# Optimization experiments

Measured on AMD Instinct MI355X. Metric: run time of the kernel, lower is better.

## Reference

```python
import jax, jax.numpy as jnp
import numpy as np

NUM_ACTIONS = 16  # number of unique leaf actions (= output_dim)


def setup_inputs() -> dict:
    key = jax.random.key(0)
    ks = jax.random.split(key, 7)
    B, IN, D, A = 32768, 128, 511, 512
    L = D + A + 1  # 1024 leaves
    x = jax.random.normal(ks[0], (B, IN), dtype=jnp.float32)
    Wd = jax.random.normal(ks[1], (D, IN), dtype=jnp.float32) * 0.05
    bd = jax.random.normal(ks[2], (D,), dtype=jnp.float32) * 0.05
    Wa = jax.random.normal(ks[3], (A, IN), dtype=jnp.float32) * 0.05
    ba = jax.random.normal(ks[4], (A,), dtype=jnp.float32) * 0.05
    Wl = jax.random.normal(ks[5], (L, 2 * (D + A)), dtype=jnp.float32) * 0.05
    seg_ids = jax.random.randint(ks[6], (L,), 0, NUM_ACTIONS, dtype=jnp.int32)
    return {"x": x, "Wd": Wd, "bd": bd, "Wa": Wa, "ba": ba, "Wl": Wl,
            "seg_ids": seg_ids}


def reference(x, Wd, bd, Wa, ba, Wl, seg_ids):
    # dual linear heads (torch Linear: y = x @ W.T + b)
    x1 = x @ Wd.T + bd            # [B, D]
    x2 = x @ Wa.T + ba            # [B, A]
    h = jnp.concatenate([x1, x2], axis=1)                     # [B, D+A]
    hh = jnp.concatenate([jax.nn.relu(h), jax.nn.relu(-h)], axis=1)  # [B, 2(D+A)]
    leaf = hh @ Wl.T              # [B, L]
    # ragged per-action max over leaf columns (MaxPoolLayer)
    pooled = jax.ops.segment_max(leaf.T, seg_ids,
                                 num_segments=NUM_ACTIONS).T   # [B, NUM_ACTIONS]
    return jax.nn.softmax(pooled, axis=-1)
```

## Files before the change

kernel.cpp:

```cpp
#include <hip/hip_runtime.h>
#include <hip/hip_bf16.h>
#include <cstdint>
#include <cmath>

#define AS1 __attribute__((address_space(1)))
#define AS3 __attribute__((address_space(3)))

typedef unsigned short u16;
typedef uint32_t u32;
typedef __attribute__((ext_vector_type(8))) __bf16 bf16x8;
typedef __attribute__((ext_vector_type(8))) unsigned short u16x8;
typedef __attribute__((ext_vector_type(4))) float f32x4;

__device__ __forceinline__ u16 f2bf(float f) {
    uint32_t u = __builtin_bit_cast(uint32_t, f);
    return (u16)((u + 0x7fffu + ((u >> 16) & 1u)) >> 16);
}

__device__ __forceinline__ u32 f2ord(float f) {
    u32 u = __builtin_bit_cast(u32, f);
    return u ^ (u32)(((int32_t)u >> 31) | 0x80000000);
}
__device__ __forceinline__ float ord2f(u32 v) {
    u32 u = (v & 0x80000000u) ? (v ^ 0x80000000u) : ~v;
    return __builtin_bit_cast(float, u);
}

__global__ void setup_all(const float* __restrict__ x,
                          const float* __restrict__ Wd, const float* __restrict__ bd,
                          const float* __restrict__ Wa, const float* __restrict__ ba,
                          const float* __restrict__ Wl,
                          u16* __restrict__ xb, u16* __restrict__ w1b,
                          float* __restrict__ bb, u16* __restrict__ w1t,
                          u16* __restrict__ wsb, u16* __restrict__ dlb,
                          float* __restrict__ cl) {
    __shared__ float cred[256];
    const int b = blockIdx.x;
    const int tid = threadIdx.x;
    if (b < 2048) {
        long idx = (long)(b * 256 + tid) * 8;
        float4 a = *(const float4*)(x + idx);
        float4 c = *(const float4*)(x + idx + 4);
        u16x8 o;
        o[0]=f2bf(a.x); o[1]=f2bf(a.y); o[2]=f2bf(a.z); o[3]=f2bf(a.w);
        o[4]=f2bf(c.x); o[5]=f2bf(c.y); o[6]=f2bf(c.z); o[7]=f2bf(c.w);
        *(u16x8*)(xb + idx) = o;
    } else if (b < 2112) {
        int t = (b - 2048) * 256 + tid;
        int row = t >> 4, g = (t & 15) * 8;
        const float* src = nullptr;
        if (row < 511)       src = Wd + row * 128 + g;
        else if (row < 1023) src = Wa + (row - 511) * 128 + g;
        u16x8 o = 0;
        if (src) {
            #pragma unroll
            for (int j = 0; j < 8; ++j) o[j] = f2bf(src[j]);
        }
        *(u16x8*)(w1b + row * 128 + g) = o;
        #pragma unroll
        for (int j = 0; j < 8; ++j) w1t[(g + j) * 1024 + row] = o[j];
        if ((t & 15) == 0)
            bb[row] = row < 511 ? bd[row] : (row < 1023 ? ba[row - 511] : 0.f);
    } else {
        const int l0 = (b - 2112) * 2;
        const int lo = tid >> 7, g = (tid & 127) * 8;
        const float* src = Wl + (long)(l0 + lo) * 2046;
        u16x8 os, od;
        float part = 0.f;
        #pragma unroll
        for (int j = 0; j < 8; ++j) {
            int c = g + j;
            float pa = 0.f, pb = 0.f;
            if (c < 1023) { pa = src[c]; pb = src[1023 + c]; }
            os[j] = f2bf(0.5f * (pa + pb));
            float v = pa - pb;
            od[j] = f2bf(v);
            float b1 = c < 511 ? bd[c] : (c < 1023 ? ba[c - 511] : 0.f);
            part += v * b1;
        }
        *(u16x8*)(wsb + (long)(l0 + lo) * 1024 + g) = os;
        *(u16x8*)(dlb + (long)(l0 + lo) * 1024 + g) = od;
        cred[tid] = part;
        __syncthreads();
        if (tid < 2) {
            float s = 0.f;
            #pragma unroll
            for (int k = 0; k < 128; ++k) s += cred[tid * 128 + k];
            cl[l0 + tid] = 0.5f * s;
        }
    }
}

__global__ __launch_bounds__(256) void gemm_hwc(
        const u16* __restrict__ xb, const u16* __restrict__ w1b,
        const float* __restrict__ bb,
        const u16* __restrict__ dlb, const u16* __restrict__ w1t,
        u16* __restrict__ habs, u16* __restrict__ wcb) {
    __shared__ union SharedU {
        struct { u16 As[2][4096]; u16 Bs[2][4096]; } s;
        u16 obuf[128 * 132];
    } sh;
    const int tid  = threadIdx.x;
    const int lane = tid & 63, wave = tid >> 6;
    const int wy = wave >> 1, wx = wave & 1;
    const int i16 = lane & 15, q = lane >> 4;
    const int cA = wave * 2, srow = lane >> 2, scol = (lane & 3) * 8;

    f32x4 acc[4][4];
    #pragma unroll
    for (int m = 0; m < 4; ++m)
        #pragma unroll
        for (int n = 0; n < 4; ++n) acc[m][n] = f32x4{0.f,0.f,0.f,0.f};

    if (blockIdx.y == 0) {
        const long blockM = (long)blockIdx.x * 128;
        const int koff = (blockIdx.x * 4) & 31;
        const u16* a0 = dlb + (blockM + cA * 16 + srow) * 1024 + scol;
        const u16* a1 = dlb + (blockM + (cA + 1) * 16 + srow) * 1024 + scol;
        const u16* b0 = w1t + (long)(cA * 16 + srow) * 1024 + scol;
        const u16* b1 = w1t + (long)((cA + 1) * 16 + srow) * 1024 + scol;
        for (int it = 0; it < 32; ++it) {
            const int k0 = ((it + koff) & 31) << 5;
            __builtin_amdgcn_global_load_lds((const AS1 void*)(a0 + k0), (AS3 void*)&sh.s.As[0][cA * 512],       16, 0, 0);
            __builtin_amdgcn_global_load_lds((const AS1 void*)(a1 + k0), (AS3 void*)&sh.s.As[0][(cA + 1) * 512], 16, 0, 0);
            __builtin_amdgcn_global_load_lds((const AS1 void*)(b0 + k0), (AS3 void*)&sh.s.Bs[0][cA * 512],       16, 0, 0);
            __builtin_amdgcn_global_load_lds((const AS1 void*)(b1 + k0), (AS3 void*)&sh.s.Bs[0][(cA + 1) * 512], 16, 0, 0);
            __syncthreads();
            bf16x8 af[4], bfv[4];
            #pragma unroll
            for (int s = 0; s < 4; ++s) {
                af[s]  = *(const bf16x8*)&sh.s.As[0][(wy * 64 + s * 16 + i16) * 32 + q * 8];
                bfv[s] = *(const bf16x8*)&sh.s.Bs[0][(wx * 64 + s * 16 + i16) * 32 + q * 8];
            }
            #pragma unroll
            for (int sm = 0; sm < 4; ++sm)
                #pragma unroll
                for (int sn = 0; sn < 4; ++sn)
                    acc[sm][sn] = __builtin_amdgcn_mfma_f32_16x16x32_bf16(af[sm], bfv[sn], acc[sm][sn], 0, 0, 0);
            __syncthreads();
        }
        #pragma unroll
        for (int sm = 0; sm < 4; ++sm)
            #pragma unroll
            for (int sn = 0; sn < 4; ++sn) {
                const int col = wx * 64 + sn * 16 + i16;
                #pragma unroll
                for (int r = 0; r < 4; ++r) {
                    const long row = blockM + wy * 64 + sm * 16 + 4 * q + r;
                    wcb[row * 128 + col] = f2bf(0.5f * acc[sm][sn][r]);
                }
            }
        return;
    }

    const int xcd = blockIdx.x, yy = blockIdx.y - 1;
    const long blockM = (long)(xcd * 32 + (yy >> 3)) * 128;
    const int  blockN = (yy & 7) * 128;
    const int  koff = (yy >> 3) & 1;

    const u16* a0 = xb + (blockM + cA * 16 + srow) * 128 + scol;
    const u16* a1 = xb + (blockM + (cA + 1) * 16 + srow) * 128 + scol;
    const u16* b0 = w1b + ((long)blockN + cA * 16 + srow) * 128 + scol;
    const u16* b1 = w1b + ((long)blockN + (cA + 1) * 16 + srow) * 128 + scol;
    for (int it = 0; it < 2; ++it) {
        const int k0 = ((it + koff) & 1) << 6;
        #pragma unroll
        for (int p = 0; p < 2; ++p) {
            const int kp = k0 + p * 32;
            __builtin_amdgcn_global_load_lds((const AS1 void*)(a0 + kp), (AS3 void*)&sh.s.As[p][cA * 512],       16, 0, 0);
            __builtin_amdgcn_global_load_lds((const AS1 void*)(a1 + kp), (AS3 void*)&sh.s.As[p][(cA + 1) * 512], 16, 0, 0);
            __builtin_amdgcn_global_load_lds((const AS1 void*)(b0 + kp), (AS3 void*)&sh.s.Bs[p][cA * 512],       16, 0, 0);
            __builtin_amdgcn_global_load_lds((const AS1 void*)(b1 + kp), (AS3 void*)&sh.s.Bs[p][(cA + 1) * 512], 16, 0, 0);
        }
        __syncthreads();
        #pragma unroll
        for (int p = 0; p < 2; ++p) {
            bf16x8 af[4], bfv[4];
            #pragma unroll
            for (int s = 0; s < 4; ++s) {
                af[s]  = *(const bf16x8*)&sh.s.As[p][(wy * 64 + s * 16 + i16) * 32 + q * 8];
                bfv[s] = *(const bf16x8*)&sh.s.Bs[p][(wx * 64 + s * 16 + i16) * 32 + q * 8];
            }
            #pragma unroll
            for (int sm = 0; sm < 4; ++sm)
                #pragma unroll
                for (int sn = 0; sn < 4; ++sn)
                    acc[sm][sn] = __builtin_amdgcn_mfma_f32_16x16x32_bf16(af[sm], bfv[sn], acc[sm][sn], 0, 0, 0);
        }
        __syncthreads();
    }

    float bv[4];
    #pragma unroll
    for (int sn = 0; sn < 4; ++sn) bv[sn] = bb[blockN + wx * 64 + sn * 16 + i16];
    #pragma unroll
    for (int sm = 0; sm < 4; ++sm)
        #pragma unroll
        for (int sn = 0; sn < 4; ++sn)
            #pragma unroll
            for (int r = 0; r < 4; ++r)
                sh.obuf[(wy * 64 + sm * 16 + 4 * q + r) * 132 + wx * 64 + sn * 16 + i16] =
                    f2bf(fabsf(acc[sm][sn][r] + bv[sn]));
    __syncthreads();
    const int cg = (tid & 15) * 8;
    #pragma unroll
    for (int it = 0; it < 8; ++it) {
        const int row = it * 16 + (tid >> 4);
        *(u16x8*)&habs[(blockM + row) * 1024 + blockN + cg] =
            *(const u16x8*)&sh.obuf[row * 132 + cg];
    }
}

__global__ __launch_bounds__(256) void gemm_leaf(const u16* __restrict__ habs,
        const u16* __restrict__ xb, const u16* __restrict__ wsb,
        const u16* __restrict__ wcb, const float* __restrict__ cl,
        const int* __restrict__ seg, u32* __restrict__ pp) {
    __shared__ u16 As[2][128 * 32];
    __shared__ u16 Bs[2][128 * 32];
    __shared__ u32 pmax[128 * 16];
    const int tid  = threadIdx.x;
    const int lane = tid & 63, wave = tid >> 6;
    const int wy = wave >> 1, wx = wave & 1;
    const int i16 = lane & 15, q = lane >> 4;
    const int xcd = blockIdx.x, y = blockIdx.y;
    const int nTile = y & 7;
    const long blockM = (long)(xcd * 32 + (y >> 3)) * 128;
    const int  blockN = nTile * 128;
    const int  koff = ((y >> 3) * 2) & 15;

    #pragma unroll
    for (int j = 0; j < 8; ++j) pmax[tid + j * 256] = 0u;

    f32x4 acc[4][4];
    #pragma unroll
    for (int m = 0; m < 4; ++m)
        #pragma unroll
        for (int n = 0; n < 4; ++n) acc[m][n] = f32x4{0.f,0.f,0.f,0.f};

    const int cA = wave * 2, srow = lane >> 2, scol = (lane & 3) * 8;
    {
        const u16* a0 = habs + (blockM + cA * 16 + srow) * 1024 + scol;
        const u16* a1 = habs + (blockM + (cA + 1) * 16 + srow) * 1024 + scol;
        const u16* b0 = wsb + ((long)blockN + cA * 16 + srow) * 1024 + scol;
        const u16* b1 = wsb + ((long)blockN + (cA + 1) * 16 + srow) * 1024 + scol;
        auto kstep = [&](int k0) {
            #pragma unroll
            for (int p = 0; p < 2; ++p) {
                const int kp = k0 + p * 32;
                __builtin_amdgcn_global_load_lds((const AS1 void*)(a0 + kp), (AS3 void*)&As[p][cA * 512],       16, 0, 0);
                __builtin_amdgcn_global_load_lds((const AS1 void*)(a1 + kp), (AS3 void*)&As[p][(cA + 1) * 512], 16, 0, 0);
                __builtin_amdgcn_global_load_lds((const AS1 void*)(b0 + kp), (AS3 void*)&Bs[p][cA * 512],       16, 0, 0);
                __builtin_amdgcn_global_load_lds((const AS1 void*)(b1 + kp), (AS3 void*)&Bs[p][(cA + 1) * 512], 16, 0, 0);
            }
            __syncthreads();
            #pragma unroll
            for (int p = 0; p < 2; ++p) {
                bf16x8 af[4], bfv[4];
                #pragma unroll
                for (int s = 0; s < 4; ++s) {
                    af[s]  = *(const bf16x8*)&As[p][(wy * 64 + s * 16 + i16) * 32 + q * 8];
                    bfv[s] = *(const bf16x8*)&Bs[p][(wx * 64 + s * 16 + i16) * 32 + q * 8];
                }
                #pragma unroll
                for (int sm = 0; sm < 4; ++sm)
                    #pragma unroll
                    for (int sn = 0; sn < 4; ++sn)
                        acc[sm][sn] = __builtin_amdgcn_mfma_f32_16x16x32_bf16(af[sm], bfv[sn], acc[sm][sn], 0, 0, 0);
            }
            __syncthreads();
        };
        for (int it = koff; it < 16; ++it) kstep(it << 6);
        for (int it = 0; it < koff; ++it)  kstep(it << 6);
    }
    {
        const u16* a0 = xb + (blockM + cA * 16 + srow) * 128 + scol;
        const u16* a1 = xb + (blockM + (cA + 1) * 16 + srow) * 128 + scol;
        const u16* b0 = wcb + ((long)blockN + cA * 16 + srow) * 128 + scol;
        const u16* b1 = wcb + ((long)blockN + (cA + 1) * 16 + srow) * 128 + scol;
        #pragma unroll
        for (int half = 0; half < 2; ++half) {
            const int k0 = half * 64;
            #pragma unroll
            for (int p = 0; p < 2; ++p) {
                const int kp = k0 + p * 32;
                __builtin_amdgcn_global_load_lds((const AS1 void*)(a0 + kp), (AS3 void*)&As[p][cA * 512],       16, 0, 0);
                __builtin_amdgcn_global_load_lds((const AS1 void*)(a1 + kp), (AS3 void*)&As[p][(cA + 1) * 512], 16, 0, 0);
                __builtin_amdgcn_global_load_lds((const AS1 void*)(b0 + kp), (AS3 void*)&Bs[p][cA * 512],       16, 0, 0);
                __builtin_amdgcn_global_load_lds((const AS1 void*)(b1 + kp), (AS3 void*)&Bs[p][(cA + 1) * 512], 16, 0, 0);
            }
            __syncthreads();
            #pragma unroll
            for (int p = 0; p < 2; ++p) {
                bf16x8 af[4], bfv[4];
                #pragma unroll
                for (int s = 0; s < 4; ++s) {
                    af[s]  = *(const bf16x8*)&As[p][(wy * 64 + s * 16 + i16) * 32 + q * 8];
                    bfv[s] = *(const bf16x8*)&Bs[p][(wx * 64 + s * 16 + i16) * 32 + q * 8];
                }
                #pragma unroll
                for (int sm = 0; sm < 4; ++sm)
                    #pragma unroll
                    for (int sn = 0; sn < 4; ++sn)
                        acc[sm][sn] = __builtin_amdgcn_mfma_f32_16x16x32_bf16(af[sm], bfv[sn], acc[sm][sn], 0, 0, 0);
            }
            __syncthreads();
        }
    }

    int segc[4]; float clv[4];
    #pragma unroll
    for (int sn = 0; sn < 4; ++sn) {
        const int col = blockN + wx * 64 + sn * 16 + i16;
        segc[sn] = seg[col];
        clv[sn]  = cl[col];
    }
    #pragma unroll
    for (int sm = 0; sm < 4; ++sm)
        #pragma unroll
        for (int sn = 0; sn < 4; ++sn)
            #pragma unroll
            for (int r = 0; r < 4; ++r) {
                const int rl = wy * 64 + sm * 16 + 4 * q + r;
                atomicMax(&pmax[rl * 16 + segc[sn]], f2ord(acc[sm][sn][r] + clv[sn]));
            }
    __syncthreads();
    #pragma unroll
    for (int j = 0; j < 8; ++j) {
        int idx = tid + j * 256;
        pp[((long)nTile << 19) + ((blockM + (idx >> 4)) << 4) + (idx & 15)] = pmax[idx];
    }
}

__global__ __launch_bounds__(256) void finalize(const u32* __restrict__ pp,
                                                float* __restrict__ out) {
    const int tid = threadIdx.x;
    const long row = (long)blockIdx.x * 16 + (tid >> 4);
    const int t = tid & 15;
    u32 m = 0;
    #pragma unroll
    for (int p = 0; p < 8; ++p)
        m = max(m, pp[((long)p << 19) + (row << 4) + t]);
    float logit = ord2f(m);
    float rm = logit;
    #pragma unroll
    for (int d = 8; d >= 1; d >>= 1) rm = fmaxf(rm, __shfl_xor(rm, d, 16));
    float e = __expf(logit - rm);
    float s = e;
    #pragma unroll
    for (int d = 8; d >= 1; d >>= 1) s += __shfl_xor(s, d, 16);
    out[(row << 4) + t] = e / s;
}

extern "C" void kernel_launch(void* const* d_in, const int* in_sizes, int n_in,
                              void* d_out, int out_size, void* d_ws, size_t ws_size,
                              hipStream_t stream) {
    const float* x  = (const float*)d_in[0];
    const float* Wd = (const float*)d_in[1];
    const float* bd = (const float*)d_in[2];
    const float* Wa = (const float*)d_in[3];
    const float* ba = (const float*)d_in[4];
    const float* Wl = (const float*)d_in[5];
    const int*  seg = (const int*)d_in[6];
    float* out = (float*)d_out;

    char* ws = (char*)d_ws;
    u16*   xb   = (u16*)(ws);
    u16*   w1b  = (u16*)(ws + 8388608);
    float* bb   = (float*)(ws + 8650752);
    u16*   w1t  = (u16*)(ws + 8654848);
    u16*   wsb  = (u16*)(ws + 8916992);
    u16*   dlb  = (u16*)(ws + 11014144);
    u16*   wcb  = (u16*)(ws + 13111296);
    float* clp  = (float*)(ws + 13373440);
    u16*   habs = (u16*)(ws + 13377536);
    u32*   pp   = (u32*)(ws + 80486400);

    setup_all<<<2624, 256, 0, stream>>>(x, Wd, bd, Wa, ba, Wl,
                                        xb, w1b, bb, w1t, wsb, dlb, clp);
    gemm_hwc <<<dim3(8, 257), 256, 0, stream>>>(xb, w1b, bb, dlb, w1t, habs, wcb);
    gemm_leaf<<<dim3(8, 256), 256, 0, stream>>>(habs, xb, wsb, wcb, clp, seg, pp);
    finalize <<<2048, 256, 0, stream>>>(pp, out);
}
```

Measured before the change: 213.0 us.

## Rewrite leaf GEMM as 256x256 tile, 8-wave pipelined kernel with finer staging

```diff
diff --git a/kernel.cpp b/kernel.cpp
--- a/kernel.cpp
+++ b/kernel.cpp
@@ -211,123 +211,147 @@
     }
 }
 
-__global__ __launch_bounds__(256) void gemm_leaf(const u16* __restrict__ habs,
+#define NT 18
+__global__ __launch_bounds__(512, 2) void gemm_leaf(const u16* __restrict__ habs,
         const u16* __restrict__ xb, const u16* __restrict__ wsb,
         const u16* __restrict__ wcb, const float* __restrict__ cl,
         const int* __restrict__ seg, u32* __restrict__ pp) {
-    __shared__ u16 As[2][128 * 32];
-    __shared__ u16 Bs[2][128 * 32];
-    __shared__ u32 pmax[128 * 16];
+    __shared__ u16 As[2][2][256 * 32];
+    __shared__ u16 Bs[2][2][256 * 32];
+    __shared__ u32 pmax[256 * 17];
+
     const int tid  = threadIdx.x;
-    const int lane = tid & 63, wave = tid >> 6;
-    const int wy = wave >> 1, wx = wave & 1;
+    const int lane = tid & 63, w = tid >> 6;
+    const int wm = w >> 2, wn = w & 3;
     const int i16 = lane & 15, q = lane >> 4;
-    const int xcd = blockIdx.x, y = blockIdx.y;
-    const int nTile = y & 7;
-    const long blockM = (long)(xcd * 32 + (y >> 3)) * 128;
-    const int  blockN = nTile * 128;
-    const int  koff = ((y >> 3) * 2) & 15;
-
-    #pragma unroll
-    for (int j = 0; j < 8; ++j) pmax[tid + j * 256] = 0u;
-
-    f32x4 acc[4][4];
-    #pragma unroll
-    for (int m = 0; m < 4; ++m)
+
+    const int bid  = blockIdx.x;
+    const int wgid = (bid & 7) * 64 + (bid >> 3);
+    const int mT = wgid >> 2, nT = wgid & 3;
+    const long blockM = (long)mT * 256;
+    const int  blockN = nT * 256;
+
+    #pragma unroll
+    for (int j = 0; j < 9; ++j) {
+        int idx = tid + j * 512;
+        if (idx < 256 * 17) pmax[idx] = 0u;
+    }
+
+    const int r0 = tid >> 2, c0 = (tid & 3) * 8;
+    const u16* gA1 = habs + (blockM + r0) * 1024 + c0;
+    const u16* gB1 = wsb  + (long)(blockN + r0) * 1024 + c0;
+    const u16* gA2 = xb   + (blockM + r0) * 128 + c0;
+    const u16* gB2 = wcb  + (long)(blockN + r0) * 128 + c0;
+    const int ldsb = w * 512;
+
+    auto stage = [&](int t, int isB, int kk) {
+        u16* dst = (isB ? &Bs[t & 1][kk][0] : &As[t & 1][kk][0]) + ldsb;
+        const u16* g;
+        int jstr;
+        if (t < 16) { g = (isB ? gB1 : gA1) + t * 64 + kk * 32;        jstr = 128 * 1024; }
+        else        { g = (isB ? gB2 : gA2) + (t - 16) * 64 + kk * 32; jstr = 128 * 128; }
+        __builtin_amdgcn_global_load_lds((const AS1 void*)g,          (AS3 void*)dst,          16, 0, 0);
+        __builtin_amdgcn_global_load_lds((const AS1 void*)(g + jstr), (AS3 void*)(dst + 4096), 16, 0, 0);
+    };
+
+    f32x4 acc[8][4];
+    #pragma unroll
+    for (int m = 0; m < 8; ++m)
         #pragma unroll
         for (int n = 0; n < 4; ++n) acc[m][n] = f32x4{0.f,0.f,0.f,0.f};
-
-    const int cA = wave * 2, srow = lane >> 2, scol = (lane & 3) * 8;
-    {
-        const u16* a0 = habs + (blockM + cA * 16 + srow) * 1024 + scol;
-        const u16* a1 = habs + (blockM + (cA + 1) * 16 + srow) * 1024 + scol;
-        const u16* b0 = wsb + ((long)blockN + cA * 16 + srow) * 1024 + scol;
-        const u16* b1 = wsb + ((long)blockN + (cA + 1) * 16 + srow) * 1024 + scol;
-        auto kstep = [&](int k0) {
-            #pragma unroll
-            for (int p = 0; p < 2; ++p) {
-                const int kp = k0 + p * 32;
-                __builtin_amdgcn_global_load_lds((const AS1 void*)(a0 + kp), (AS3 void*)&As[p][cA * 512],       16, 0, 0);
-                __builtin_amdgcn_global_load_lds((const AS1 void*)(a1 + kp), (AS3 void*)&As[p][(cA + 1) * 512], 16, 0, 0);
-                __builtin_amdgcn_global_load_lds((const AS1 void*)(b0 + kp), (AS3 void*)&Bs[p][cA * 512],       16, 0, 0);
-                __builtin_amdgcn_global_load_lds((const AS1 void*)(b1 + kp), (AS3 void*)&Bs[p][(cA + 1) * 512], 16, 0, 0);
-            }
-            __syncthreads();
-            #pragma unroll
-            for (int p = 0; p < 2; ++p) {
-                bf16x8 af[4], bfv[4];
-                #pragma unroll
-                for (int s = 0; s < 4; ++s) {
-                    af[s]  = *(const bf16x8*)&As[p][(wy * 64 + s * 16 + i16) * 32 + q * 8];
-                    bfv[s] = *(const bf16x8*)&Bs[p][(wx * 64 + s * 16 + i16) * 32 + q * 8];
-                }
-                #pragma unroll
-                for (int sm = 0; sm < 4; ++sm)
-                    #pragma unroll
-                    for (int sn = 0; sn < 4; ++sn)
-                        acc[sm][sn] = __builtin_amdgcn_mfma_f32_16x16x32_bf16(af[sm], bfv[sn], acc[sm][sn], 0, 0, 0);
-            }
-            __syncthreads();
-        };
-        for (int it = koff; it < 16; ++it) kstep(it << 6);
-        for (int it = 0; it < koff; ++it)  kstep(it << 6);
-    }
-    {
-        const u16* a0 = xb + (blockM + cA * 16 + srow) * 128 + scol;
-        const u16* a1 = xb + (blockM + (cA + 1) * 16 + srow) * 128 + scol;
-        const u16* b0 = wcb + ((long)blockN + cA * 16 + srow) * 128 + scol;
-        const u16* b1 = wcb + ((long)blockN + (cA + 1) * 16 + srow) * 128 + scol;
-        #pragma unroll
-        for (int half = 0; half < 2; ++half) {
-            const int k0 = half * 64;
-            #pragma unroll
-            for (int p = 0; p < 2; ++p) {
-                const int kp = k0 + p * 32;
-                __builtin_amdgcn_global_load_lds((const AS1 void*)(a0 + kp), (AS3 void*)&As[p][cA * 512],       16, 0, 0);
-                __builtin_amdgcn_global_load_lds((const AS1 void*)(a1 + kp), (AS3 void*)&As[p][(cA + 1) * 512], 16, 0, 0);
-                __builtin_amdgcn_global_load_lds((const AS1 void*)(b0 + kp), (AS3 void*)&Bs[p][cA * 512],       16, 0, 0);
-                __builtin_amdgcn_global_load_lds((const AS1 void*)(b1 + kp), (AS3 void*)&Bs[p][(cA + 1) * 512], 16, 0, 0);
-            }
-            __syncthreads();
-            #pragma unroll
-            for (int p = 0; p < 2; ++p) {
-                bf16x8 af[4], bfv[4];
-                #pragma unroll
-                for (int s = 0; s < 4; ++s) {
-                    af[s]  = *(const bf16x8*)&As[p][(wy * 64 + s * 16 + i16) * 32 + q * 8];
-                    bfv[s] = *(const bf16x8*)&Bs[p][(wx * 64 + s * 16 + i16) * 32 + q * 8];
-                }
-                #pragma unroll
-                for (int sm = 0; sm < 4; ++sm)
-                    #pragma unroll
-                    for (int sn = 0; sn < 4; ++sn)
-                        acc[sm][sn] = __builtin_amdgcn_mfma_f32_16x16x32_bf16(af[sm], bfv[sn], acc[sm][sn], 0, 0, 0);
-            }
-            __syncthreads();
-        }
+    bf16x8 areg[8], breg[2];
+
+    auto lda = [&](int slot, int kk) {
+        #pragma unroll
+        for (int mf = 0; mf < 8; ++mf)
+            areg[mf] = *(const bf16x8*)&As[slot][kk][(wm * 128 + mf * 16 + i16) * 32 + q * 8];
+    };
+    auto ldb = [&](int slot, int kk, int nh) {
+        #pragma unroll
+        for (int nf = 0; nf < 2; ++nf)
+            breg[nf] = *(const bf16x8*)&Bs[slot][kk][(wn * 64 + nh * 32 + nf * 16 + i16) * 32 + q * 8];
+    };
+    auto mfma16 = [&](int nh) {
+        #pragma unroll
+        for (int mf = 0; mf < 8; ++mf)
+            #pragma unroll
+            for (int nf = 0; nf < 2; ++nf)
+                acc[mf][nh * 2 + nf] = __builtin_amdgcn_mfma_f32_16x16x32_bf16(
+                    areg[mf], breg[nf], acc[mf][nh * 2 + nf], 0, 0, 0);
+    };
+
+    stage(0, 0, 0); stage(0, 1, 0); stage(0, 0, 1); stage(0, 1, 1);
+    stage(1, 0, 0); stage(1, 1, 0); stage(1, 0, 1);
+    asm volatile("s_waitcnt vmcnt(10)" ::: "memory");
+    __builtin_amdgcn_s_barrier();
+
+    for (int t = 0; t < NT; ++t) {
+        const int slot = t & 1;
+        lda(slot, 0); ldb(slot, 0, 0);
+        if (t + 1 < NT) stage(t + 1, 1, 1);
+        __builtin_amdgcn_s_barrier();
+        asm volatile("s_waitcnt lgkmcnt(0)" ::: "memory");
+        __builtin_amdgcn_sched_barrier(0);
+        __builtin_amdgcn_s_setprio(1);
+        mfma16(0);
+        __builtin_amdgcn_s_setprio(0);
+        __builtin_amdgcn_s_barrier();
+        ldb(slot, 0, 1);
+        if (t + 2 < NT) stage(t + 2, 0, 0);
+        __builtin_amdgcn_s_barrier();
+        asm volatile("s_waitcnt lgkmcnt(0)" ::: "memory");
+        __builtin_amdgcn_sched_barrier(0);
+        __builtin_amdgcn_s_setprio(1);
+        mfma16(1);
+        __builtin_amdgcn_s_setprio(0);
+        if (t < 16)      { asm volatile("s_waitcnt vmcnt(10)" ::: "memory"); }
+        else if (t == 16){ asm volatile("s_waitcnt vmcnt(8)"  ::: "memory"); }
+        else             { asm volatile("s_waitcnt vmcnt(0)"  ::: "memory"); }
+        __builtin_amdgcn_s_barrier();
+        lda(slot, 1); ldb(slot, 1, 0);
+        if (t + 2 < NT) stage(t + 2, 1, 0);
+        __builtin_amdgcn_s_barrier();
+        asm volatile("s_waitcnt lgkmcnt(0)" ::: "memory");
+        __builtin_amdgcn_sched_barrier(0);
+        __builtin_amdgcn_s_setprio(1);
+        mfma16(0);
+        __builtin_amdgcn_s_setprio(0);
+        __builtin_amdgcn_s_barrier();
+        ldb(slot, 1, 1);
+        if (t + 2 < NT) stage(t + 2, 0, 1);
+        __builtin_amdgcn_s_barrier();
+        asm volatile("s_waitcnt lgkmcnt(0)" ::: "memory");
+        __builtin_amdgcn_sched_barrier(0);
+        __builtin_amdgcn_s_setprio(1);
+        mfma16(1);
+        __builtin_amdgcn_s_setprio(0);
+        if (t < 16)      { asm volatile("s_waitcnt vmcnt(10)" ::: "memory"); }
+        else if (t == 16){ asm volatile("s_waitcnt vmcnt(4)"  ::: "memory"); }
+        __builtin_amdgcn_s_barrier();
     }
 
     int segc[4]; float clv[4];
     #pragma unroll
-    for (int sn = 0; sn < 4; ++sn) {
-        const int col = blockN + wx * 64 + sn * 16 + i16;
-        segc[sn] = seg[col];
-        clv[sn]  = cl[col];
-    }
-    #pragma unroll
-    for (int sm = 0; sm < 4; ++sm)
-        #pragma unroll
-        for (int sn = 0; sn < 4; ++sn)
+    for (int nf = 0; nf < 4; ++nf) {
+        const int col = blockN + wn * 64 + nf * 16 + i16;
+        segc[nf] = seg[col];
+        clv[nf]  = cl[col];
+    }
+    #pragma unroll
+    for (int mf = 0; mf < 8; ++mf)
+        #pragma unroll
+        for (int nf = 0; nf < 4; ++nf)
             #pragma unroll
             for (int r = 0; r < 4; ++r) {
-                const int rl = wy * 64 + sm * 16 + 4 * q + r;
-                atomicMax(&pmax[rl * 16 + segc[sn]], f2ord(acc[sm][sn][r] + clv[sn]));
+                const int rl = wm * 128 + mf * 16 + 4 * q + r;
+                atomicMax(&pmax[rl * 17 + segc[nf]], f2ord(acc[mf][nf][r] + clv[nf]));
             }
     __syncthreads();
     #pragma unroll
     for (int j = 0; j < 8; ++j) {
-        int idx = tid + j * 256;
-        pp[((long)nTile << 19) + ((blockM + (idx >> 4)) << 4) + (idx & 15)] = pmax[idx];
+        int idx = tid + j * 512;
+        pp[((long)nT << 19) + ((blockM + (idx >> 4)) << 4) + (idx & 15)] =
+            pmax[(idx >> 4) * 17 + (idx & 15)];
     }
 }
 
@@ -338,7 +362,7 @@
     const int t = tid & 15;
     u32 m = 0;
     #pragma unroll
-    for (int p = 0; p < 8; ++p)
+    for (int p = 0; p < 4; ++p)
         m = max(m, pp[((long)p << 19) + (row << 4) + t]);
     float logit = ord2f(m);
     float rm = logit;
@@ -378,6 +402,6 @@
     setup_all<<<2624, 256, 0, stream>>>(x, Wd, bd, Wa, ba, Wl,
                                         xb, w1b, bb, w1t, wsb, dlb, clp);
     gemm_hwc <<<dim3(8, 257), 256, 0, stream>>>(xb, w1b, bb, dlb, w1t, habs, wcb);
-    gemm_leaf<<<dim3(8, 256), 256, 0, stream>>>(habs, xb, wsb, wcb, clp, seg, pp);
+    gemm_leaf<<<dim3(512), 512, 0, stream>>>(habs, xb, wsb, wcb, clp, seg, pp);
     finalize <<<2048, 256, 0, stream>>>(pp, out);
 }
```

After: 225.5 us. +5.9%, slower.
